# Optimization experiments

Hardware: AMD Instinct MI355X
Metric: run time of the kernel (lower is better)

## Reference

```python
import jax, jax.numpy as jnp
import numpy as np

# init_kwargs (closed over, matching BaseDepthVolumeModel.__init__)
DEPTH_START = 0.5
DEPTH_END = 10.0
DEPTH_NUM = 64

N_SAMPLES, N_VIEWS, HEIGHT, WIDTH = 2, 4, 256, 320


def _make_extrinsics(key, shape):
    """Random small-rotation-about-y + translation world->camera 4x4 matrices."""
    ang = jax.random.uniform(key, shape, minval=-0.2, maxval=0.2)
    c, s = jnp.cos(ang), jnp.sin(ang)
    z, o = jnp.zeros_like(ang), jnp.ones_like(ang)
    R = jnp.stack([c, z, s, z, o, z, -s, z, c], axis=-1).reshape(*shape, 3, 3)
    t = jax.random.uniform(jax.random.fold_in(key, 1), (*shape, 3), minval=-0.5, maxval=0.5)
    E = jnp.zeros((*shape, 4, 4), jnp.float32)
    E = E.at[..., :3, :3].set(R).at[..., :3, 3].set(t).at[..., 3, 3].set(1.0)
    return E.astype(jnp.float32)


def setup_inputs() -> dict:
    key = jax.random.key(0)
    k1, k2 = jax.random.split(key)
    fx = fy = 200.0
    K = jnp.array([[fx, 0.0, WIDTH / 2.0], [0.0, fy, HEIGHT / 2.0], [0.0, 0.0, 1.0]], jnp.float32)
    return {
        "dst_intrinsics": jnp.broadcast_to(K, (N_SAMPLES, 1, 3, 3)),
        "dst_extrinsics": _make_extrinsics(k1, (N_SAMPLES, 1)),
        "src_intrinsics": jnp.broadcast_to(K, (N_SAMPLES, N_VIEWS, 3, 3)),
        "src_extrinsics": _make_extrinsics(k2, (N_SAMPLES, N_VIEWS)),
        "n_samples": N_SAMPLES,
        "n_views": N_VIEWS,
        "height": HEIGHT,
        "width": WIDTH,
    }


def reference(dst_intrinsics, dst_extrinsics, src_intrinsics, src_extrinsics,
              n_samples, n_views, height, width):
    # Plane-sweep target->source projection for every (sample, view, depth, pixel),
    # fully batched instead of the original triple Python loop.
    depths = jnp.linspace(DEPTH_START, DEPTH_END, DEPTH_NUM).astype(jnp.float32)  # [D]

    Kd = dst_intrinsics[:, 0]                       # [N,3,3]
    Ed = dst_extrinsics[:, 0]                       # [N,4,4]
    # relative transform source_cam <- target_cam:  T = E_src @ inv(E_dst)
    T = jnp.einsum('nvij,njk->nvik', src_extrinsics, jnp.linalg.inv(Ed))  # [N,V,4,4]
    R, t = T[..., :3, :3], T[..., :3, 3]
    A = jnp.einsum('nvij,nvjk->nvik', src_intrinsics, R)                  # K_src @ R  [N,V,3,3]
    b = jnp.einsum('nvij,nvj->nvi', src_intrinsics, t)                    # K_src @ t  [N,V,3]

    # homogeneous pixel grid of the target view, [H,W,3]
    xs = jnp.arange(width, dtype=jnp.float32)
    ys = jnp.arange(height, dtype=jnp.float32)
    X, Y = jnp.meshgrid(xs, ys, indexing='xy')
    grid_h = jnp.stack([X, Y, jnp.ones_like(X)], axis=-1)                 # [H,W,3]

    rays = jnp.einsum('nij,hwj->nhwi', jnp.linalg.inv(Kd), grid_h)        # K_dst^-1 p  [N,H,W,3]
    base = jnp.einsum('nvij,nhwj->nvhwi', A, rays)                        # [N,V,H,W,3]
    # proj = d * (K_src R K_dst^-1 p) + K_src t  -> [N,V,D,H,W,3]
    proj = depths[None, None, :, None, None, None] * base[:, :, None] + b[:, :, None, None, None, :]

    z = proj[..., 2:3]
    z_safe = jnp.where(jnp.abs(z) < 1e-8, 1e-8, z)
    xy = proj[..., :2] / z_safe                                           # source pixel coords

    in_x = (xy[..., 0:1] >= 0.0) & (xy[..., 0:1] <= width - 1)
    in_y = (xy[..., 1:2] >= 0.0) & (xy[..., 1:2] <= height - 1)
    mask = (in_x & in_y & (z > 0.0)).astype(jnp.float32)                  # [N,V,D,H,W,1]

    return xy, mask
```

## Files before the change

### kernel.cpp

```cpp
#include <hip/hip_runtime.h>
#include <math.h>

#define N_S 2
#define N_V 4
#define DQ  64
#define HH  256
#define WW  320
#define HW  (HH * WW)
#define SPLIT 8
#define CHUNK_PX (HW / SPLIT)
#define ITERS (CHUNK_PX / (256 * 2))

typedef float f32x4 __attribute__((ext_vector_type(4)));
typedef float f32x2 __attribute__((ext_vector_type(2)));

__global__ __launch_bounds__(256) void slice_kernel(
    const float* __restrict__ Kd,
    const float* __restrict__ Ed,
    const float* __restrict__ Ks,
    const float* __restrict__ Es,
    float* __restrict__ out)
{
    int bid   = blockIdx.x;
    int chunk = bid % SPLIT;
    int d     = (bid / SPLIT) % DQ;
    int nv    = bid / (SPLIT * DQ);
    int n     = nv >> 2;

    const float* E = Ed + n * 16;
    float Ri[3][3], ti[3];
    #pragma unroll
    for (int r = 0; r < 3; ++r)
        #pragma unroll
        for (int c = 0; c < 3; ++c)
            Ri[r][c] = E[c * 4 + r];
    #pragma unroll
    for (int r = 0; r < 3; ++r)
        ti[r] = -(Ri[r][0] * E[3] + Ri[r][1] * E[7] + Ri[r][2] * E[11]);

    const float* S = Es + nv * 16;
    float Tr[3][3], Tt[3];
    #pragma unroll
    for (int r = 0; r < 3; ++r) {
        #pragma unroll
        for (int c = 0; c < 3; ++c)
            Tr[r][c] = S[r*4+0]*Ri[0][c] + S[r*4+1]*Ri[1][c] + S[r*4+2]*Ri[2][c];
        Tt[r] = S[r*4+0]*ti[0] + S[r*4+1]*ti[1] + S[r*4+2]*ti[2] + S[r*4+3];
    }

    const float* Kv = Ks + nv * 9;
    float Am[3][3], bm[3];
    #pragma unroll
    for (int r = 0; r < 3; ++r) {
        #pragma unroll
        for (int c = 0; c < 3; ++c)
            Am[r][c] = Kv[r*3+0]*Tr[0][c] + Kv[r*3+1]*Tr[1][c] + Kv[r*3+2]*Tr[2][c];
        bm[r] = Kv[r*3+0]*Tt[0] + Kv[r*3+1]*Tt[1] + Kv[r*3+2]*Tt[2];
    }

    float IK[3][3];
    {
        const float* Km = Kd + n * 9;
        float a=Km[0],b=Km[1],c=Km[2],dd=Km[3],e=Km[4],f=Km[5],g=Km[6],hh=Km[7],k=Km[8];
        float det = a*(e*k - f*hh) - b*(dd*k - f*g) + c*(dd*hh - e*g);
        float inv = 1.0f / det;
        IK[0][0] =  (e*k - f*hh) * inv;
        IK[0][1] = -(b*k - c*hh) * inv;
        IK[0][2] =  (b*f - c*e) * inv;
        IK[1][0] = -(dd*k - f*g) * inv;
        IK[1][1] =  (a*k - c*g) * inv;
        IK[1][2] = -(a*f - c*dd) * inv;
        IK[2][0] =  (dd*hh - e*g) * inv;
        IK[2][1] = -(a*hh - b*g) * inv;
        IK[2][2] =  (a*e - b*dd) * inv;
    }

    const float step = (float)(9.5 / 63.0);
    float depth = 0.5f + (float)d * step;
    float Q[3][3], cvec[3];
    #pragma unroll
    for (int r = 0; r < 3; ++r) {
        #pragma unroll
        for (int c = 0; c < 3; ++c)
            Q[r][c] = depth * (Am[r][0]*IK[0][c] + Am[r][1]*IK[1][c] + Am[r][2]*IK[2][c]);
        cvec[r] = Q[r][2] + bm[r];
    }
    float Q00=Q[0][0], Q01=Q[0][1], c0=cvec[0];
    float Q10=Q[1][0], Q11=Q[1][1], c1=cvec[1];
    float Q20=Q[2][0], Q21=Q[2][1], c2=cvec[2];

    size_t slice = (size_t)nv * DQ + (size_t)d;
    float* __restrict__ xyp = out + slice * (size_t)HW * 2 + (size_t)chunk * CHUNK_PX * 2;
    float* __restrict__ mp  = out + (size_t)N_S * N_V * DQ * HW * 2
                            + slice * (size_t)HW + (size_t)chunk * CHUNK_PX;

    int t2 = threadIdx.x * 2;
    int gbase = chunk * CHUNK_PX + t2;

    #pragma unroll 4
    for (int j = 0; j < ITERS; ++j) {
        int pix  = j * 512 + t2;
        int gpix = gbase + j * 512;
        int h = gpix / WW;
        int w = gpix - h * WW;
        float X = (float)w, Y = (float)h;

        float px0 = Q00*X + Q01*Y + c0;
        float py0 = Q10*X + Q11*Y + c1;
        float pz0 = Q20*X + Q21*Y + c2;
        float px1 = px0 + Q00;
        float py1 = py0 + Q10;
        float pz1 = pz0 + Q20;

        float zs0 = (fabsf(pz0) < 1e-8f) ? 1e-8f : pz0;
        float zs1 = (fabsf(pz1) < 1e-8f) ? 1e-8f : pz1;
        float r0 = __builtin_amdgcn_rcpf(zs0);
        r0 = r0 * (2.0f - zs0 * r0);
        float r1 = __builtin_amdgcn_rcpf(zs1);
        r1 = r1 * (2.0f - zs1 * r1);

        float x0 = px0 * r0, y0 = py0 * r0;
        float x1 = px1 * r1, y1 = py1 * r1;

        float m0 = (x0 >= 0.0f && x0 <= (float)(WW-1) &&
                    y0 >= 0.0f && y0 <= (float)(HH-1) && pz0 > 0.0f) ? 1.0f : 0.0f;
        float m1 = (x1 >= 0.0f && x1 <= (float)(WW-1) &&
                    y1 >= 0.0f && y1 <= (float)(HH-1) && pz1 > 0.0f) ? 1.0f : 0.0f;

        f32x4 xyv; xyv.x = x0; xyv.y = y0; xyv.z = x1; xyv.w = y1;
        __builtin_nontemporal_store(xyv, (f32x4*)(xyp + (size_t)pix * 2));
        f32x2 mv; mv.x = m0; mv.y = m1;
        __builtin_nontemporal_store(mv, (f32x2*)(mp + pix));
    }
}

extern "C" void kernel_launch(void* const* d_in, const int* in_sizes, int n_in,
                              void* d_out, int out_size, void* d_ws, size_t ws_size,
                              hipStream_t stream) {
    const float* Kd = (const float*)d_in[0];
    const float* Ed = (const float*)d_in[1];
    const float* Ks = (const float*)d_in[2];
    const float* Es = (const float*)d_in[3];

    int blocks = N_S * N_V * DQ * SPLIT;
    hipLaunchKernelGGL(slice_kernel, dim3(blocks), dim3(256), 0, stream,
                       Kd, Ed, Ks, Es, (float*)d_out);
}
```

Before: 102.1 us.

## Split xy and mask outputs into separate block sets with wider mask stores

Blocks are split into two groups: one writes only the xy coordinates and the other recomputes the projection to write only the mask, using 16-byte stores of four mask values per thread instead of 8-byte stores. Pixel row/column indices are now advanced incrementally rather than recomputed with a division each iteration. The aim is to make each block's write stream contiguous and vectorised, which should improve memory-write efficiency on a store-bound kernel. In exchange, the projection and reciprocal math run twice and the grid doubles in size.

```diff
diff --git a/kernel.cpp b/kernel.cpp
--- a/kernel.cpp
+++ b/kernel.cpp
@@ -9,24 +9,20 @@
 #define HW  (HH * WW)
 #define SPLIT 8
 #define CHUNK_PX (HW / SPLIT)
-#define ITERS (CHUNK_PX / (256 * 2))
+#define XY_ITERS (CHUNK_PX / 512)
+#define MK_ITERS (CHUNK_PX / 1024)
+
+#define XY_BLOCKS (N_S * N_V * DQ * SPLIT)
+#define TOT_BLOCKS (2 * XY_BLOCKS)
 
 typedef float f32x4 __attribute__((ext_vector_type(4)));
-typedef float f32x2 __attribute__((ext_vector_type(2)));
 
-__global__ __launch_bounds__(256) void slice_kernel(
-    const float* __restrict__ Kd,
-    const float* __restrict__ Ed,
-    const float* __restrict__ Ks,
-    const float* __restrict__ Es,
-    float* __restrict__ out)
+__device__ __forceinline__ void camera_setup_folded(
+    const float* __restrict__ Kd, const float* __restrict__ Ed,
+    const float* __restrict__ Ks, const float* __restrict__ Es,
+    int nv, int n, int d,
+    float Q[3][3], float cvec[3])
 {
-    int bid   = blockIdx.x;
-    int chunk = bid % SPLIT;
-    int d     = (bid / SPLIT) % DQ;
-    int nv    = bid / (SPLIT * DQ);
-    int n     = nv >> 2;
-
     const float* E = Ed + n * 16;
     float Ri[3][3], ti[3];
     #pragma unroll
@@ -77,7 +73,6 @@
 
     const float step = (float)(9.5 / 63.0);
     float depth = 0.5f + (float)d * step;
-    float Q[3][3], cvec[3];
     #pragma unroll
     for (int r = 0; r < 3; ++r) {
         #pragma unroll
@@ -85,52 +80,88 @@
             Q[r][c] = depth * (Am[r][0]*IK[0][c] + Am[r][1]*IK[1][c] + Am[r][2]*IK[2][c]);
         cvec[r] = Q[r][2] + bm[r];
     }
-    float Q00=Q[0][0], Q01=Q[0][1], c0=cvec[0];
-    float Q10=Q[1][0], Q11=Q[1][1], c1=cvec[1];
-    float Q20=Q[2][0], Q21=Q[2][1], c2=cvec[2];
+}
+
+__global__ __launch_bounds__(256) void stream_kernel(
+    const float* __restrict__ Kd, const float* __restrict__ Ed,
+    const float* __restrict__ Ks, const float* __restrict__ Es,
+    float* __restrict__ out)
+{
+    int bid = blockIdx.x;
+    bool is_mask = (bid >= XY_BLOCKS);
+    int rb = is_mask ? (bid - XY_BLOCKS) : bid;
+
+    int chunk = rb % SPLIT;
+    int d     = (rb / SPLIT) % DQ;
+    int nv    = rb / (SPLIT * DQ);
+    int n     = nv >> 2;
+
+    float Q[3][3], cv[3];
+    camera_setup_folded(Kd, Ed, Ks, Es, nv, n, d, Q, cv);
+    float Q00=Q[0][0], Q01=Q[0][1], c0=cv[0];
+    float Q10=Q[1][0], Q11=Q[1][1], c1=cv[1];
+    float Q20=Q[2][0], Q21=Q[2][1], c2=cv[2];
 
     size_t slice = (size_t)nv * DQ + (size_t)d;
-    float* __restrict__ xyp = out + slice * (size_t)HW * 2 + (size_t)chunk * CHUNK_PX * 2;
-    float* __restrict__ mp  = out + (size_t)N_S * N_V * DQ * HW * 2
-                            + slice * (size_t)HW + (size_t)chunk * CHUNK_PX;
 
-    int t2 = threadIdx.x * 2;
-    int gbase = chunk * CHUNK_PX + t2;
+    if (!is_mask) {
+        float* __restrict__ xyp = out + (slice * (size_t)HW + (size_t)chunk * CHUNK_PX) * 2;
+        int t2 = threadIdx.x * 2;
+        int pix0 = chunk * CHUNK_PX + t2;
+        int h = pix0 / WW;
+        int w = pix0 - h * WW;
 
-    #pragma unroll 4
-    for (int j = 0; j < ITERS; ++j) {
-        int pix  = j * 512 + t2;
-        int gpix = gbase + j * 512;
-        int h = gpix / WW;
-        int w = gpix - h * WW;
-        float X = (float)w, Y = (float)h;
+        #pragma unroll 4
+        for (int j = 0; j < XY_ITERS; ++j) {
+            float X = (float)w, Y = (float)h;
+            float px0 = Q00*X + Q01*Y + c0;
+            float py0 = Q10*X + Q11*Y + c1;
+            float pz0 = Q20*X + Q21*Y + c2;
+            float px1 = px0 + Q00, py1 = py0 + Q10, pz1 = pz0 + Q20;
 
-        float px0 = Q00*X + Q01*Y + c0;
-        float py0 = Q10*X + Q11*Y + c1;
-        float pz0 = Q20*X + Q21*Y + c2;
-        float px1 = px0 + Q00;
-        float py1 = py0 + Q10;
-        float pz1 = pz0 + Q20;
+            float zs0 = (fabsf(pz0) < 1e-8f) ? 1e-8f : pz0;
+            float zs1 = (fabsf(pz1) < 1e-8f) ? 1e-8f : pz1;
+            float r0 = __builtin_amdgcn_rcpf(zs0); r0 = r0 * (2.0f - zs0 * r0);
+            float r1 = __builtin_amdgcn_rcpf(zs1); r1 = r1 * (2.0f - zs1 * r1);
 
-        float zs0 = (fabsf(pz0) < 1e-8f) ? 1e-8f : pz0;
-        float zs1 = (fabsf(pz1) < 1e-8f) ? 1e-8f : pz1;
-        float r0 = __builtin_amdgcn_rcpf(zs0);
-        r0 = r0 * (2.0f - zs0 * r0);
-        float r1 = __builtin_amdgcn_rcpf(zs1);
-        r1 = r1 * (2.0f - zs1 * r1);
+            f32x4 xyv;
+            xyv.x = px0 * r0; xyv.y = py0 * r0;
+            xyv.z = px1 * r1; xyv.w = py1 * r1;
+            __builtin_nontemporal_store(xyv, (f32x4*)(xyp + (size_t)(j * 512 + t2) * 2));
 
-        float x0 = px0 * r0, y0 = py0 * r0;
-        float x1 = px1 * r1, y1 = py1 * r1;
+            w += 192; h += 1;
+            if (w >= WW) { w -= WW; h += 1; }
+        }
+    } else {
+        float* __restrict__ mp = out + (size_t)N_S * N_V * DQ * HW * 2
+                               + slice * (size_t)HW + (size_t)chunk * CHUNK_PX;
+        int t4 = threadIdx.x * 4;
+        int pix0 = chunk * CHUNK_PX + t4;
+        int h = pix0 / WW;
+        int w = pix0 - h * WW;
 
-        float m0 = (x0 >= 0.0f && x0 <= (float)(WW-1) &&
-                    y0 >= 0.0f && y0 <= (float)(HH-1) && pz0 > 0.0f) ? 1.0f : 0.0f;
-        float m1 = (x1 >= 0.0f && x1 <= (float)(WW-1) &&
-                    y1 >= 0.0f && y1 <= (float)(HH-1) && pz1 > 0.0f) ? 1.0f : 0.0f;
+        #pragma unroll 2
+        for (int j = 0; j < MK_ITERS; ++j) {
+            float X = (float)w, Y = (float)h;
+            float px = Q00*X + Q01*Y + c0;
+            float py = Q10*X + Q11*Y + c1;
+            float pz = Q20*X + Q21*Y + c2;
 
-        f32x4 xyv; xyv.x = x0; xyv.y = y0; xyv.z = x1; xyv.w = y1;
-        __builtin_nontemporal_store(xyv, (f32x4*)(xyp + (size_t)pix * 2));
-        f32x2 mv; mv.x = m0; mv.y = m1;
-        __builtin_nontemporal_store(mv, (f32x2*)(mp + pix));
+            f32x4 mv;
+            #pragma unroll
+            for (int p = 0; p < 4; ++p) {
+                float zs = (fabsf(pz) < 1e-8f) ? 1e-8f : pz;
+                float r  = __builtin_amdgcn_rcpf(zs); r = r * (2.0f - zs * r);
+                float x = px * r, y = py * r;
+                mv[p] = (x >= 0.0f && x <= (float)(WW-1) &&
+                         y >= 0.0f && y <= (float)(HH-1) && pz > 0.0f) ? 1.0f : 0.0f;
+                px += Q00; py += Q10; pz += Q20;
+            }
+            __builtin_nontemporal_store(mv, (f32x4*)(mp + (size_t)(j * 1024 + t4)));
+
+            w += 64; h += 3;
+            if (w >= WW) { w -= WW; h += 1; }
+        }
     }
 }
 
@@ -142,7 +173,6 @@
     const float* Ks = (const float*)d_in[2];
     const float* Es = (const float*)d_in[3];
 
-    int blocks = N_S * N_V * DQ * SPLIT;
-    hipLaunchKernelGGL(slice_kernel, dim3(blocks), dim3(256), 0, stream,
+    hipLaunchKernelGGL(stream_kernel, dim3(TOT_BLOCKS), dim3(256), 0, stream,
                        Kd, Ed, Ks, Es, (float*)d_out);
 }
```

After: 105.9 us. 3.7% more time.
